# Kernel optimization log

Measured on AMD Instinct MI355X. Metric: run time of the kernel, lower is better.

The kernel has to match this reference:

```python
import jax, jax.numpy as jnp
import numpy as np

N, C_IN, T, V, M = 2048, 16, 8, 21, 2
C_OUT = 64
VM = V * M                       # 42 = n_joints
NUM_NODES = N * T * VM           # 688128 flattened nodes
NUM_HEDGES = NUM_NODES           # hyperedge ids drawn from same range
E_INC = 4 * NUM_NODES            # incidence (node, hyperedge) pairs
EMBED = VM * C_OUT // 8          # 336
HEADS = 4
HEAD_DIM = EMBED // HEADS        # 84


def setup_inputs() -> dict:
    key = jax.random.key(0)
    ks = jax.random.split(key, 16)
    g = lambda k, s: jax.random.normal(k, s, jnp.float32) * 0.02
    return dict(
        x=jax.random.normal(ks[0], (N, C_IN, T, V, M), jnp.float32),
        hi=jax.random.randint(ks[1], (2, E_INC), 0, NUM_NODES, jnp.int32),
        hc_w=g(ks[2], (C_OUT, C_IN)), hc_b=jnp.zeros((C_OUT,), jnp.float32),
        conv_w=g(ks[3], (8, 8)), conv_b=jnp.zeros((8,), jnp.float32),
        bn_gamma=jnp.ones((C_IN,), jnp.float32), bn_beta=jnp.zeros((C_IN,), jnp.float32),
        proj_w=g(ks[4], (C_OUT, C_IN)), proj_b=jnp.zeros((C_OUT,), jnp.float32),
        wq=g(ks[5], (EMBED, EMBED)), bq=jnp.zeros((EMBED,), jnp.float32),
        wk=g(ks[6], (EMBED, EMBED)), bk=jnp.zeros((EMBED,), jnp.float32),
        wv=g(ks[7], (EMBED, EMBED)), bv=jnp.zeros((EMBED,), jnp.float32),
        in_proj_w=g(ks[8], (3 * EMBED, EMBED)), in_proj_b=jnp.zeros((3 * EMBED,), jnp.float32),
        out_proj_w=g(ks[9], (EMBED, EMBED)), out_proj_b=jnp.zeros((EMBED,), jnp.float32),
        fc_w=g(ks[10], (8 * EMBED, EMBED)), fc_b=jnp.zeros((8 * EMBED,), jnp.float32),
    )


def _forward(x, hi, hc_w, hc_b, conv_w, conv_b, bn_gamma, bn_beta, proj_w, proj_b,
             wq, bq, wk, bk, wv, bv, in_proj_w, in_proj_b, out_proj_w, out_proj_b,
             fc_w, fc_b):
    # ---- residual branch: rearrange n c t v m -> n c (vm) t, BN (train-mode batch stats), proj ----
    res = x.reshape(N, C_IN, T, VM).transpose(0, 1, 3, 2)          # [N,C,VM,T]
    mean = res.mean(axis=(0, 2, 3), keepdims=True)
    var = ((res - mean) ** 2).mean(axis=(0, 2, 3), keepdims=True)
    res = (res - mean) * jax.lax.rsqrt(var + 1e-5)
    res = res * bn_gamma[None, :, None, None] + bn_beta[None, :, None, None]
    res = res.transpose(0, 3, 2, 1)                                 # n t vm c
    res = res @ proj_w.T + proj_b                                   # [N,T,VM,C_OUT]
    res = res.reshape(N, T, VM * C_OUT)                             # [N,8,2688]

    # ---- HypergraphConv (PyG math: D^-1 H B H^T X Theta + bias) ----
    xn = x.transpose(0, 2, 3, 4, 1).reshape(NUM_NODES, C_IN)        # (n t v m) c
    xt = xn @ hc_w.T                                                # [Nn, C_OUT]
    node_idx, edge_idx = hi[0], hi[1]
    ones = jnp.ones((E_INC,), xt.dtype)
    D = jax.ops.segment_sum(ones, node_idx, NUM_NODES)
    Dinv = jnp.where(D > 0, 1.0 / D, 0.0)
    Bd = jax.ops.segment_sum(ones, edge_idx, NUM_HEDGES)
    Binv = jnp.where(Bd > 0, 1.0 / Bd, 0.0)
    e = jax.ops.segment_sum(Binv[edge_idx, None] * xt[node_idx], edge_idx, NUM_HEDGES)
    h = jax.ops.segment_sum(Dinv[node_idx, None] * e[edge_idx], node_idx, NUM_NODES)
    h = h + hc_b                                                    # [Nn, C_OUT]

    # torch .view(N,-1,T,V,M) is a raw reshape of the (nodes, C) buffer
    h = h.reshape(N, C_OUT, T, V, M)
    h = h.transpose(0, 2, 3, 4, 1).reshape(N, T, VM, C_OUT)         # n t vm c

    # ---- Conv2d(8->8, k=(1,1), stride=(1,8)) over channel dim T ----
    hs = h[:, :, :, ::8]                                            # [N,8,VM,8]
    hc2 = jnp.einsum('oi,nivw->novw', conv_w, hs) + conv_b[None, :, None, None]
    seq = hc2.transpose(0, 1, 3, 2).reshape(N, 8, EMBED)            # n t (c vm) -> [N,8,336]

    # ---- external QKV projections + nn.MultiheadAttention ----
    q = seq @ wq.T + bq
    k = seq @ wk.T + bk
    v = seq @ wv.T + bv
    qq = q @ in_proj_w[:EMBED].T + in_proj_b[:EMBED]
    kk = k @ in_proj_w[EMBED:2 * EMBED].T + in_proj_b[EMBED:2 * EMBED]
    vv = v @ in_proj_w[2 * EMBED:].T + in_proj_b[2 * EMBED:]
    qq = qq.reshape(N, 8, HEADS, HEAD_DIM)
    kk = kk.reshape(N, 8, HEADS, HEAD_DIM)
    vv = vv.reshape(N, 8, HEADS, HEAD_DIM)
    scores = jnp.einsum('nshd,nthd->nhst', qq, kk) / np.sqrt(HEAD_DIM).astype(np.float32)
    attn = jax.nn.softmax(scores, axis=-1)
    ao = jnp.einsum('nhst,nthd->nshd', attn, vv).reshape(N, 8, EMBED)
    ao = ao @ out_proj_w.T + out_proj_b

    out = ao @ fc_w.T + fc_b                                        # [N,8,8*EMBED=2688]
    out = jax.nn.relu(out + res)
    return out.reshape(N, 64, T, V, M)                              # raw view, C'=64


def reference(x, hi, hc_w, hc_b, conv_w, conv_b, bn_gamma, bn_beta, proj_w, proj_b,
              wq, bq, wk, bk, wv, bv, in_proj_w, in_proj_b, out_proj_w, out_proj_b,
              fc_w, fc_b):
    return _forward(x, hi, hc_w, hc_b, conv_w, conv_b, bn_gamma, bn_beta, proj_w, proj_b,
                    wq, bq, wk, bk, wv, bv, in_proj_w, in_proj_b, out_proj_w, out_proj_b,
                    fc_w, fc_b)
```

## Files before the change

kernel.cpp:

```cpp
#include <hip/hip_runtime.h>

#define N_    2048
#define CIN   16
#define T_    8
#define VM_   42
#define COUT  64
#define NODES (N_*T_*VM_)
#define EINC  (4*NODES)
#define EMB   336
#define PERN  (T_*VM_*COUT)
#define XPERN (CIN*T_*VM_)
#define NBUK  672
#define BCAP  4608
#define LCAP  16

typedef __attribute__((ext_vector_type(8))) short bf16x8;
typedef __attribute__((ext_vector_type(4))) float f32x4;
typedef unsigned short ushort_t;
typedef unsigned char  uchar_t;

static const size_t O_A   = 0;
static const size_t SZ_AB = (size_t)NODES*64;
static const size_t O_B   = SZ_AB;
static const size_t O_SEQ = 2*SZ_AB;
static const size_t SZ_SEQ= (size_t)N_*8*EMB;
static const size_t O_AO  = O_SEQ+SZ_SEQ;
static const size_t O_SD  = O_AO+SZ_SEQ;
static const size_t O_BN  = O_SD + 4*(size_t)NODES;
static const size_t O_BE  = O_BN + 64;
static const size_t O_WF  = O_BE + 4096;
static const size_t O_SEQF = O_B;
static const size_t O_AOF  = O_B + 3600000;
static const size_t O_QKV  = O_B + 6600000;

__device__ inline short bf16r(float f){
    unsigned u = __builtin_bit_cast(unsigned, f);
    u += 0x7FFFu + ((u>>16)&1u);
    return (short)(u>>16);
}
__device__ inline float b2f(ushort_t u){
    return __builtin_bit_cast(float, ((unsigned)u)<<16);
}
__device__ inline uchar_t f2fp8(float f){
    return (uchar_t)(__builtin_amdgcn_cvt_pk_fp8_f32(f,f,0,false)&0xFFu);
}

__global__ __launch_bounds__(256) void k_bn_stats(const float* __restrict__ x, float* __restrict__ bn){
    int b=blockIdx.x, ci=b&15, grp=b>>4;
    int w=threadIdx.x>>6, lane=threadIdx.x&63;
    float s=0.f,q=0.f;
    for(int i=0;i<16;i++){
        int n = grp*64 + w*16 + i;
        const float4* r4 = (const float4*)(x + (size_t)n*XPERN + ci*336);
        for(int k=lane;k<84;k+=64){
            float4 v=r4[k];
            s += v.x+v.y+v.z+v.w;
            q += v.x*v.x+v.y*v.y+v.z*v.z+v.w*v.w;
        }
    }
    for(int off=32;off;off>>=1){ s+=__shfl_down(s,off); q+=__shfl_down(q,off); }
    if(lane==0){ atomicAdd(bn+ci,s); atomicAdd(bn+16+ci,q); }
}

__global__ void k_bn_final(float* bn, const float* __restrict__ g, const float* __restrict__ b){
    int c = threadIdx.x;
    if(c<16){
        const float inv = 1.f/(float)NODES;
        float mean = bn[c]*inv;
        float var  = bn[16+c]*inv - mean*mean;
        float rs   = rsqrtf(var+1e-5f);
        float sc   = g[c]*rs;
        bn[32+c] = sc;
        bn[48+c] = b[c]-mean*sc;
    }
}

__global__ __launch_bounds__(256) void k_xt(const float* __restrict__ x, const float* __restrict__ hcw, uchar_t* __restrict__ xt){
    __shared__ float xs[5376];
    int n=blockIdx.x, tid=threadIdx.x;
    const float4* xr4=(const float4*)(x+(size_t)n*XPERN);
    float4* xs4=(float4*)xs;
    for(int f=tid; f<1344; f+=256) xs4[f]=xr4[f];
    int co=tid&63, q=tid>>6;
    float w[16];
    #pragma unroll
    for(int ci=0;ci<16;ci++) w[ci]=hcw[co*16+ci];
    __syncthreads();
    uchar_t* xn = xt + (size_t)n*336*64;
    for(int g=0; g<21; g++){
        int tl0 = q*84 + g*4;
        float4 acc={0.f,0.f,0.f,0.f};
        #pragma unroll
        for(int ci=0;ci<16;ci++){
            float4 xv = *(const float4*)(xs + ci*336 + tl0);
            acc.x+=xv.x*w[ci]; acc.y+=xv.y*w[ci]; acc.z+=xv.z*w[ci]; acc.w+=xv.w*w[ci];
        }
        xn[(size_t)(tl0+0)*64+co]=f2fp8(acc.x);
        xn[(size_t)(tl0+1)*64+co]=f2fp8(acc.y);
        xn[(size_t)(tl0+2)*64+co]=f2fp8(acc.z);
        xn[(size_t)(tl0+3)*64+co]=f2fp8(acc.w);
    }
}

__global__ void k_initcur(int* __restrict__ gcurE, int* __restrict__ gcurD){
    int i=blockIdx.x*256+threadIdx.x;
    if(i<NBUK){ gcurE[i]=i*BCAP; gcurD[i]=i*BCAP; }
}

__global__ __launch_bounds__(256) void k_bin(const int* __restrict__ seg, const int* __restrict__ pay,
                                             int* __restrict__ gcur, unsigned* __restrict__ staging){
    __shared__ unsigned bins[NBUK*LCAP];
    __shared__ int lcnt[NBUK];
    int tid=threadIdx.x;
    for(int i=tid;i<NBUK;i+=256) lcnt[i]=0;
    __syncthreads();
    int base=blockIdx.x*4096;
    for(int k=0;k<16;k++){
        int i=base+k*256+tid;
        int sv=seg[i], pv=pay[i];
        int b=sv>>10;
        unsigned e=((unsigned)(sv&1023)<<20)|(unsigned)pv;
        int p=atomicAdd(&lcnt[b],1);
        if(p<LCAP) bins[b*LCAP+p]=e;
        else{
            int g=atomicAdd(&gcur[b],1);
            if(g<(b+1)*BCAP) staging[g]=e;
        }
    }
    __syncthreads();
    for(int b=tid;b<NBUK;b+=256){
        int c=lcnt[b]; if(c>LCAP)c=LCAP;
        if(c>0){
            int g=atomicAdd(&gcur[b],c);
            int lim=(b+1)*BCAP;
            for(int j=0;j<c;j++) if(g+j<lim) staging[g+j]=bins[b*LCAP+j];
        }
    }
}

__global__ __launch_bounds__(256) void k_csrsort(unsigned* __restrict__ staging, const int* __restrict__ gcur,
                                                 int* __restrict__ startX, int* __restrict__ cntX){
    __shared__ unsigned ents[BCAP];
    __shared__ unsigned outp[BCAP];
    __shared__ int segc[1024];
    __shared__ int wsum[4];
    int b=blockIdx.x, tid=threadIdx.x, lane=tid&63, wv=tid>>6;
    int cnt_b = gcur[b] - b*BCAP;
    if(cnt_b>BCAP) cnt_b=BCAP;
    unsigned* sb = staging + (size_t)b*BCAP;
    for(int i=tid;i<cnt_b;i+=256) ents[i]=sb[i];
    for(int i=tid;i<1024;i+=256) segc[i]=0;
    __syncthreads();
    for(int i=tid;i<cnt_b;i+=256) atomicAdd(&segc[ents[i]>>20],1);
    __syncthreads();
    int c0=segc[tid*4],c1=segc[tid*4+1],c2=segc[tid*4+2],c3=segc[tid*4+3];
    int tsum=c0+c1+c2+c3;
    int incl=tsum;
    #pragma unroll
    for(int off=1;off<64;off<<=1){ int v=__shfl_up(incl,off); if(lane>=off) incl+=v; }
    if(lane==63) wsum[wv]=incl;
    __syncthreads();
    int w0=wsum[0],w1=wsum[1],w2=wsum[2];
    int wexcl = (wv>0?w0:0)+(wv>1?w1:0)+(wv>2?w2:0);
    int run = incl - tsum + wexcl;
    int gs = b*1024 + tid*4;
    startX[gs+0]=b*BCAP+run; cntX[gs+0]=c0; segc[tid*4+0]=run; run+=c0;
    startX[gs+1]=b*BCAP+run; cntX[gs+1]=c1; segc[tid*4+1]=run; run+=c1;
    startX[gs+2]=b*BCAP+run; cntX[gs+2]=c2; segc[tid*4+2]=run; run+=c2;
    startX[gs+3]=b*BCAP+run; cntX[gs+3]=c3; segc[tid*4+3]=run; run+=c3;
    __syncthreads();
    for(int i=tid;i<cnt_b;i+=256){
        unsigned e=ents[i]; int s=e>>20;
        int p=atomicAdd(&segc[s],1);
        outp[p]=e&0xFFFFFu;
    }
    __syncthreads();
    for(int i=tid;i<cnt_b;i+=256) sb[i]=outp[i];
}

__global__ __launch_bounds__(256) void k_gath(const uchar_t* __restrict__ src, const int* __restrict__ csr,
                                              const int* __restrict__ startX, const int* __restrict__ cntX,
                                              uchar_t* __restrict__ dst){
    int s = blockIdx.x*8 + (threadIdx.x>>5);
    int l = threadIdx.x & 31;
    int c = cntX[s];
    int start = startX[s];
    float ax=0.f, ay=0.f;
    int nv = (c<32)? c : 32;
    int myidx = (l<nv)? csr[start+l] : 0;
    for(int j=0;j<nv;j++){
        int idx = __shfl(myidx, j, 32);
        unsigned v = *(const ushort_t*)(src + (size_t)idx*64 + l*2);
        ax += __builtin_amdgcn_cvt_f32_fp8(v,0);
        ay += __builtin_amdgcn_cvt_f32_fp8(v,1);
    }
    for(int j=32;j<c;j++){
        int idx = csr[start+j];
        unsigned v = *(const ushort_t*)(src + (size_t)idx*64 + l*2);
        ax += __builtin_amdgcn_cvt_f32_fp8(v,0);
        ay += __builtin_amdgcn_cvt_f32_fp8(v,1);
    }
    float scale = (c>0)? 1.f/(float)c : 0.f;
    unsigned p = __builtin_amdgcn_cvt_pk_fp8_f32(ax*scale, ay*scale, 0, false);
    *(ushort_t*)(dst + (size_t)s*64 + l*2) = (ushort_t)(p&0xFFFFu);
}

__global__ __launch_bounds__(256) void k_seq(const uchar_t* __restrict__ h,
                                             const float* __restrict__ hcb, const float* __restrict__ cw,
                                             const float* __restrict__ cb, short* __restrict__ seqf){
    __shared__ float hb[64], cws[64], cbs[8];
    int n = blockIdx.x, tid=threadIdx.x;
    if(tid<64){ hb[tid]=hcb[tid]; cws[tid]=cw[tid]; }
    if(tid<8) cbs[tid]=cb[tid];
    __syncthreads();
    const uchar_t* hn = h + (size_t)n*PERN;
    int rbase = (n&1)*8;
    short* d0 = seqf + (size_t)(n>>1)*5632;
    for(int e=tid; e<336; e+=256){
        int k = e/42, u = e%42;
        float hv[8];
        #pragma unroll
        for(int t=0;t<8;t++){
            int idx = 2688*k + t*42 + u;
            hv[t] = __builtin_amdgcn_cvt_f32_fp8((unsigned)hn[idx],0) + hb[idx&63];
        }
        int lpart = ((e>>3)&3)<<4;
        size_t obase = (size_t)(e>>5)*512 + (e&7);
        #pragma unroll
        for(int o=0;o<8;o++){
            float acc=cbs[o];
            #pragma unroll
            for(int t=0;t<8;t++) acc += cws[o*8+t]*hv[t];
            d0[obase + (size_t)((rbase+o)|lpart)*8] = bf16r(acc);
        }
    }
    if(tid<128){
        int o=tid>>4, kk=336+(tid&15);
        int l=(rbase+o)|(((kk>>3)&3)<<4);
        d0[(size_t)(kk>>5)*512 + (size_t)l*8 + (kk&7)] = 0;
    }
}

__global__ __launch_bounds__(256) void k_fusew2(const float* __restrict__ ipw, const float* __restrict__ ipb,
        const float* __restrict__ wq, const float* __restrict__ wk, const float* __restrict__ wv,
        const float* __restrict__ bq, const float* __restrict__ bk, const float* __restrict__ bv,
        const float* __restrict__ fcw, const float* __restrict__ opw,
        const float* __restrict__ opb, const float* __restrict__ fcb,
        short* __restrict__ W1F, short* __restrict__ W2F, float* __restrict__ BE){
    __shared__ float As[5376], Ws[5376], bms[336];
    int rt=blockIdx.x, r0=rt*16, tid=threadIdx.x;
    int m=(r0<1008)?(r0/336):3;
    const float* Asrc = (m<3)? (ipw+(size_t)r0*336) : (fcw+(size_t)(r0-1008)*336);
    const float* Bmat = (m==0)?wq:((m==1)?wk:((m==2)?wv:opw));
    const float* bvec = (m==0)?bq:((m==1)?bk:((m==2)?bv:opb));
    for(int f=tid;f<5376;f+=256) As[f]=Asrc[f];
    for(int f=tid;f<336;f+=256) bms[f]=bvec[f];
    __syncthreads();
    if(tid<168){
        int i0=tid, i1=tid+168;
        float a0[16], a1[16];
        #pragma unroll
        for(int r=0;r<16;r++){a0[r]=0.f;a1[r]=0.f;}
        for(int k=0;k<336;k++){
            float b0=Bmat[(size_t)k*336+i0];
            float b1=Bmat[(size_t)k*336+i1];
            #pragma unroll
            for(int r=0;r<16;r++){ float av=As[r*336+k]; a0[r]+=av*b0; a1[r]+=av*b1; }
        }
        #pragma unroll
        for(int r=0;r<16;r++){ Ws[r*336+i0]=a0[r]; Ws[r*336+i1]=a1[r]; }
    }
    if(tid>=192 && tid<208){
        int rr=tid-192;
        float acc=(m<3)? ipb[r0+rr] : fcb[r0+rr-1008];
        for(int k=0;k<336;k++) acc+=As[rr*336+k]*bms[k];
        BE[r0+rr]=acc;
    }
    __syncthreads();
    short* dst=(m<3)? (W1F+(size_t)rt*5632) : (W2F+(size_t)(rt-63)*5632);
    for(int f=tid; f<5632; f+=256){
        int kb=f>>9, rem=f&511, l=rem>>3, j=rem&7;
        int row=l&15, k=kb*32+((l>>4)<<3)+j;
        dst[f] = (k<336)? bf16r(Ws[row*336+k]) : (short)0;
    }
}

__global__ __launch_bounds__(256) void k_res(const float* __restrict__ x, const float* __restrict__ bn,
                                             const float* __restrict__ pw, const float* __restrict__ pb,
                                             const float* __restrict__ bfc, ushort_t* __restrict__ res){
    __shared__ float xp[5376], pws[1024], pbs[64], scs[16], shs[16];
    int n=blockIdx.x, tid=threadIdx.x;
    if(tid<16){ scs[tid]=bn[32+tid]; shs[tid]=bn[48+tid]; }
    if(tid<64) pbs[tid]=pb[tid];
    for(int f=tid;f<1024;f+=256) pws[f]=pw[f];
    __syncthreads();
    const float* xn = x + (size_t)n*XPERN;
    for(int f=tid;f<5376;f+=256){ int ci=f/336; xp[f]=xn[f]*scs[ci]+shs[ci]; }
    __syncthreads();
    ushort_t* rn = res + (size_t)n*PERN;
    for(int j=tid;j<2688;j+=256){
        int co=j&63, w=j>>6;
        float base = bfc[j]+pbs[co];
        float a[8];
        #pragma unroll
        for(int s=0;s<8;s++) a[s]=base;
        #pragma unroll
        for(int ci=0;ci<16;ci++){
            float c=pws[co*16+ci];
            const float* xr = xp + ci*336 + w;
            #pragma unroll
            for(int s=0;s<8;s++) a[s]+=c*xr[s*42];
        }
        #pragma unroll
        for(int s=0;s<8;s++) rn[s*2688+j]=(ushort_t)bf16r(a[s]);
    }
}

__global__ __launch_bounds__(256) void k_gemm_qkv(const bf16x8* __restrict__ Af, const bf16x8* __restrict__ Wf,
                                                  const float* __restrict__ bias, ushort_t* __restrict__ C){
    __shared__ float stage[32][68];
    int wv = threadIdx.x>>6, l = threadIdx.x&63;
    int ct = blockIdx.y*4 + wv;
    int rt0 = blockIdx.x*2;
    if(ct<63){
        const bf16x8* Ap = Af + (size_t)rt0*704 + l;
        const bf16x8* Bp = Wf + (size_t)ct *704 + l;
        f32x4 acc0={0.f,0.f,0.f,0.f}, acc1={0.f,0.f,0.f,0.f};
        #pragma unroll
        for(int kb=0;kb<11;kb++){
            bf16x8 b  = Bp[kb*64];
            bf16x8 a0 = Ap[kb*64];
            bf16x8 a1 = Ap[704 + kb*64];
            acc0 = __builtin_amdgcn_mfma_f32_16x16x32_bf16(a0,b,acc0,0,0,0);
            acc1 = __builtin_amdgcn_mfma_f32_16x16x32_bf16(a1,b,acc1,0,0,0);
        }
        int cc=wv*16+(l&15), rr0=(l>>4)*4;
        float bb = bias[ct*16+(l&15)];
        #pragma unroll
        for(int r=0;r<4;r++){
            stage[rr0+r][cc]    = acc0[r]+bb;
            stage[rr0+16+r][cc] = acc1[r]+bb;
        }
    }
    __syncthreads();
    int lr=threadIdx.x>>3, q=threadIdx.x&7;
    int col0 = blockIdx.y*64 + q*8;
    if(col0<1008){
        short u8[8];
        #pragma unroll
        for(int j=0;j<8;j++) u8[j]=bf16r(stage[lr][q*8+j]);
        *(bf16x8*)(C + (size_t)(rt0*16+lr)*1008 + col0) = *(bf16x8*)u8;
    }
}

__global__ __launch_bounds__(256) void k_gemm_out(const bf16x8* __restrict__ Af, const bf16x8* __restrict__ Wf,
                                                  const ushort_t* __restrict__ res, float* __restrict__ C){
    __shared__ float stage[32][68];
    int wv = threadIdx.x>>6, l = threadIdx.x&63;
    int ct = blockIdx.y*4 + wv;
    int rt0 = blockIdx.x*2;
    {
        const bf16x8* Ap = Af + (size_t)rt0*704 + l;
        const bf16x8* Bp = Wf + (size_t)ct *704 + l;
        f32x4 acc0={0.f,0.f,0.f,0.f}, acc1={0.f,0.f,0.f,0.f};
        #pragma unroll
        for(int kb=0;kb<11;kb++){
            bf16x8 b  = Bp[kb*64];
            bf16x8 a0 = Ap[kb*64];
            bf16x8 a1 = Ap[704 + kb*64];
            acc0 = __builtin_amdgcn_mfma_f32_16x16x32_bf16(a0,b,acc0,0,0,0);
            acc1 = __builtin_amdgcn_mfma_f32_16x16x32_bf16(a1,b,acc1,0,0,0);
        }
        int cc=wv*16+(l&15), rr0=(l>>4)*4;
        #pragma unroll
        for(int r=0;r<4;r++){
            stage[rr0+r][cc]    = acc0[r];
            stage[rr0+16+r][cc] = acc1[r];
        }
    }
    __syncthreads();
    int lr=threadIdx.x>>3, q=threadIdx.x&7;
    int row = rt0*16 + lr;
    int col0 = blockIdx.y*64 + q*8;
    bf16x8 rv = *(const bf16x8*)(res + (size_t)row*2688 + col0);
    float v[8];
    #pragma unroll
    for(int j=0;j<8;j++){
        float t = stage[lr][q*8+j] + b2f((ushort_t)rv[j]);
        v[j] = fmaxf(t,0.f);
    }
    float* dst = C + (size_t)row*2688 + col0;
    float4 f0={v[0],v[1],v[2],v[3]}, f1={v[4],v[5],v[6],v[7]};
    *(float4*)dst = f0;
    *(float4*)(dst+4) = f1;
}

__global__ __launch_bounds__(256) void k_attn2(const ushort_t* __restrict__ qkv, short* __restrict__ aof){
    __shared__ float ss[8*1008];
    __shared__ float sc[256];
    __shared__ float aos[8*336];
    int n=blockIdx.x, tid=threadIdx.x;
    const bf16x8* src8 = (const bf16x8*)(qkv + (size_t)n*8064);
    for(int i=tid; i<1008; i+=256){
        bf16x8 v = src8[i];
        #pragma unroll
        for(int j=0;j<8;j++) ss[i*8+j]=b2f((ushort_t)v[j]);
    }
    __syncthreads();
    {
        int h=tid>>6, s=(tid>>3)&7, t=tid&7;
        const float* qp=ss + s*1008 + h*84;
        const float* kp=ss + t*1008 + 336 + h*84;
        float d=0.f;
        for(int d0=0;d0<84;d0++) d+=qp[d0]*kp[d0];
        sc[tid]=d*0.10910894511799619f;
    }
    __syncthreads();
    if(tid<32){
        float* row = sc + (tid>>3)*64 + (tid&7)*8;
        float m=row[0];
        #pragma unroll
        for(int t=1;t<8;t++) m=fmaxf(m,row[t]);
        float sum=0.f;
        #pragma unroll
        for(int t=0;t<8;t++){ float e=__expf(row[t]-m); row[t]=e; sum+=e; }
        float r=1.f/sum;
        #pragma unroll
        for(int t=0;t<8;t++) row[t]*=r;
    }
    __syncthreads();
    for(int o=tid;o<336;o+=256){
        int h=o/84;
        float acc[8];
        #pragma unroll
        for(int s=0;s<8;s++) acc[s]=0.f;
        #pragma unroll
        for(int t=0;t<8;t++){
            float v=ss[t*1008+672+o];
            #pragma unroll
            for(int s=0;s<8;s++) acc[s]+=sc[h*64+s*8+t]*v;
        }
        #pragma unroll
        for(int s=0;s<8;s++) aos[s*336+o]=acc[s];
    }
    __syncthreads();
    int rt=n>>1, half=n&1;
    for(int e=tid; e<2816; e+=256){
        int row=e&7, k=e>>3;
        float v = (k<336)? aos[row*336+k] : 0.f;
        int l = (half*8+row) | (((k>>3)&3)<<4);
        int j = k&7;
        aof[(size_t)rt*5632 + (size_t)(k>>5)*512 + l*8 + j] = bf16r(v);
    }
}

extern "C" void kernel_launch(void* const* d_in, const int* in_sizes, int n_in,
                              void* d_out, int out_size, void* d_ws, size_t ws_size,
                              hipStream_t stream) {
    const float* x    = (const float*)d_in[0];
    const int*   hi   = (const int*  )d_in[1];
    const float* hcw  = (const float*)d_in[2];
    const float* hcb  = (const float*)d_in[3];
    const float* cw   = (const float*)d_in[4];
    const float* cb   = (const float*)d_in[5];
    const float* bng  = (const float*)d_in[6];
    const float* bnb  = (const float*)d_in[7];
    const float* pw   = (const float*)d_in[8];
    const float* pb   = (const float*)d_in[9];
    const float* wq   = (const float*)d_in[10];
    const float* bq   = (const float*)d_in[11];
    const float* wk   = (const float*)d_in[12];
    const float* bk   = (const float*)d_in[13];
    const float* wv   = (const float*)d_in[14];
    const float* bv   = (const float*)d_in[15];
    const float* ipw  = (const float*)d_in[16];
    const float* ipb  = (const float*)d_in[17];
    const float* opw  = (const float*)d_in[18];
    const float* opb  = (const float*)d_in[19];
    const float* fcw  = (const float*)d_in[20];
    const float* fcb  = (const float*)d_in[21];
    float* ws  = (float*)d_ws;
    float* out = (float*)d_out;

    unsigned* stgE = (unsigned*)(ws + O_SEQ);
    int* gcurE = (int*)(ws + O_SEQ) + (size_t)NBUK*BCAP;
    int* gcurD = gcurE + NBUK;
    unsigned* stgD = (unsigned*)(ws + O_AO);
    int* SD = (int*)(ws + O_SD);
    short* W1F = (short*)(ws + O_WF);
    short* W2F = W1F + (size_t)63*5632;
    ushort_t* qkvp = (ushort_t*)(ws + O_QKV);

    hipMemsetAsync(ws + O_BN, 0, 64*sizeof(float), stream);
    k_initcur<<<3,256,0,stream>>>(gcurE, gcurD);

    k_bn_stats<<<512,256,0,stream>>>(x, ws+O_BN);
    k_bn_final<<<1,64,0,stream>>>(ws+O_BN, bng, bnb);
    k_xt<<<2048,256,0,stream>>>(x, hcw, (uchar_t*)(ws+O_A));
    k_fusew2<<<231,256,0,stream>>>(ipw, ipb, wq, wk, wv, bq, bk, bv,
                                   fcw, opw, opb, fcb, W1F, W2F, ws+O_BE);

    k_bin<<<NBUK,256,0,stream>>>(hi+EINC, hi, gcurE, stgE);
    k_bin<<<NBUK,256,0,stream>>>(hi, hi+EINC, gcurD, stgD);
    k_csrsort<<<NBUK,256,0,stream>>>(stgE, gcurE, SD, SD+NODES);
    k_csrsort<<<NBUK,256,0,stream>>>(stgD, gcurD, SD+2*(size_t)NODES, SD+3*(size_t)NODES);

    k_gath<<<86016,256,0,stream>>>((const uchar_t*)(ws+O_A), (const int*)stgE,
                                   SD, SD+NODES, (uchar_t*)(ws+O_B));
    k_gath<<<86016,256,0,stream>>>((const uchar_t*)(ws+O_B), (const int*)stgD,
                                   SD+2*(size_t)NODES, SD+3*(size_t)NODES, (uchar_t*)(ws+O_A));

    k_seq<<<2048,256,0,stream>>>((const uchar_t*)(ws+O_A), hcb, cw, cb, (short*)(ws+O_SEQF));
    k_res<<<2048,256,0,stream>>>(x, ws+O_BN, pw, pb, ws+O_BE+1008, (ushort_t*)(ws+O_A));
    {   dim3 g1(512,16);
        k_gemm_qkv<<<g1,256,0,stream>>>((const bf16x8*)(ws+O_SEQF),(const bf16x8*)W1F,
                                        ws+O_BE, qkvp); }
    k_attn2<<<2048,256,0,stream>>>(qkvp, (short*)(ws+O_AOF));
    {   dim3 g2(512,42);
        k_gemm_out<<<g2,256,0,stream>>>((const bf16x8*)(ws+O_AOF),(const bf16x8*)W2F,
                                        (const ushort_t*)(ws+O_A), out); }
}
```

Baseline: 1.018 ms.

## Keep weight tiles in registers and double-buffer A rows through LDS in GEMMs

Both MFMA GEMM kernels now load each wave's 16-column weight tile into registers once and loop over 16 row tiles per block, prefetching the next A tile into a double-buffered LDS array. This is meant to cut redundant global loads of weights and A across many small blocks. The LDS-staged vectorized epilogue is replaced by direct scalar stores per lane, which may reduce store coalescing on the large fp32 output, and the grid shrinks to fewer, larger blocks.

New measurement: 938.0 us. 7.8% less time.

```diff
diff --git a/kernel.cpp b/kernel.cpp
--- a/kernel.cpp
+++ b/kernel.cpp
@@ -316,83 +316,107 @@
     }
 }
 
-__global__ __launch_bounds__(256) void k_gemm_qkv(const bf16x8* __restrict__ Af, const bf16x8* __restrict__ Wf,
+__global__ __launch_bounds__(512) void k_gemm_qkv(const bf16x8* __restrict__ Af, const bf16x8* __restrict__ Wf,
                                                   const float* __restrict__ bias, ushort_t* __restrict__ C){
-    __shared__ float stage[32][68];
-    int wv = threadIdx.x>>6, l = threadIdx.x&63;
-    int ct = blockIdx.y*4 + wv;
-    int rt0 = blockIdx.x*2;
-    if(ct<63){
-        const bf16x8* Ap = Af + (size_t)rt0*704 + l;
-        const bf16x8* Bp = Wf + (size_t)ct *704 + l;
-        f32x4 acc0={0.f,0.f,0.f,0.f}, acc1={0.f,0.f,0.f,0.f};
-        #pragma unroll
-        for(int kb=0;kb<11;kb++){
-            bf16x8 b  = Bp[kb*64];
-            bf16x8 a0 = Ap[kb*64];
-            bf16x8 a1 = Ap[704 + kb*64];
-            acc0 = __builtin_amdgcn_mfma_f32_16x16x32_bf16(a0,b,acc0,0,0,0);
-            acc1 = __builtin_amdgcn_mfma_f32_16x16x32_bf16(a1,b,acc1,0,0,0);
-        }
-        int cc=wv*16+(l&15), rr0=(l>>4)*4;
-        float bb = bias[ct*16+(l&15)];
-        #pragma unroll
-        for(int r=0;r<4;r++){
-            stage[rr0+r][cc]    = acc0[r]+bb;
-            stage[rr0+16+r][cc] = acc1[r]+bb;
-        }
-    }
-    __syncthreads();
-    int lr=threadIdx.x>>3, q=threadIdx.x&7;
-    int col0 = blockIdx.y*64 + q*8;
-    if(col0<1008){
-        short u8[8];
-        #pragma unroll
-        for(int j=0;j<8;j++) u8[j]=bf16r(stage[lr][q*8+j]);
-        *(bf16x8*)(C + (size_t)(rt0*16+lr)*1008 + col0) = *(bf16x8*)u8;
-    }
-}
-
-__global__ __launch_bounds__(256) void k_gemm_out(const bf16x8* __restrict__ Af, const bf16x8* __restrict__ Wf,
+    __shared__ short as[2][5632];
+    int tid=threadIdx.x, wid=tid>>6, l=tid&63;
+    int ct = blockIdx.y*8 + wid;
+    bool act = (ct<63);
+    bf16x8 Breg[11];
+    if(act){
+        const bf16x8* Bp = Wf + (size_t)ct*704 + l;
+        #pragma unroll
+        for(int kb=0;kb<11;kb++) Breg[kb]=Bp[kb*64];
+    }
+    float bb = act ? bias[ct*16+(l&15)] : 0.f;
+    int rt0 = blockIdx.x*16;
+    {
+        const bf16x8* src = Af + (size_t)rt0*704;
+        bf16x8 p0 = src[tid];
+        *(bf16x8*)&as[0][tid*8] = p0;
+        if(tid<192){ bf16x8 p1 = src[512+tid]; *(bf16x8*)&as[0][(512+tid)*8] = p1; }
+    }
+    __syncthreads();
+    for(int i=0;i<16;i++){
+        bf16x8 q0, q1;
+        bool pf = (i+1<16);
+        if(pf){
+            const bf16x8* src = Af + (size_t)(rt0+i+1)*704;
+            q0 = src[tid];
+            if(tid<192) q1 = src[512+tid];
+        }
+        f32x4 acc={0.f,0.f,0.f,0.f};
+        if(act){
+            const short* ab = as[i&1];
+            #pragma unroll
+            for(int kb=0;kb<11;kb++){
+                bf16x8 a = *(const bf16x8*)&ab[(kb*64+l)*8];
+                acc = __builtin_amdgcn_mfma_f32_16x16x32_bf16(a,Breg[kb],acc,0,0,0);
+            }
+            int row0 = (rt0+i)*16 + (l>>4)*4;
+            int col  = ct*16 + (l&15);
+            #pragma unroll
+            for(int rr=0;rr<4;rr++)
+                C[(size_t)(row0+rr)*1008 + col] = (ushort_t)bf16r(acc[rr]+bb);
+        }
+        if(pf){
+            *(bf16x8*)&as[(i+1)&1][tid*8] = q0;
+            if(tid<192) *(bf16x8*)&as[(i+1)&1][(512+tid)*8] = q1;
+        }
+        __syncthreads();
+    }
+}
+
+__global__ __launch_bounds__(512) void k_gemm_out(const bf16x8* __restrict__ Af, const bf16x8* __restrict__ Wf,
                                                   const ushort_t* __restrict__ res, float* __restrict__ C){
-    __shared__ float stage[32][68];
-    int wv = threadIdx.x>>6, l = threadIdx.x&63;
-    int ct = blockIdx.y*4 + wv;
-    int rt0 = blockIdx.x*2;
+    __shared__ short as[2][5632];
+    int tid=threadIdx.x, wid=tid>>6, l=tid&63;
+    int ct = blockIdx.y*8 + wid;
+    bf16x8 Breg[11];
     {
-        const bf16x8* Ap = Af + (size_t)rt0*704 + l;
-        const bf16x8* Bp = Wf + (size_t)ct *704 + l;
-        f32x4 acc0={0.f,0.f,0.f,0.f}, acc1={0.f,0.f,0.f,0.f};
-        #pragma unroll
-        for(int kb=0;kb<11;kb++){
-            bf16x8 b  = Bp[kb*64];
-            bf16x8 a0 = Ap[kb*64];
-            bf16x8 a1 = Ap[704 + kb*64];
-            acc0 = __builtin_amdgcn_mfma_f32_16x16x32_bf16(a0,b,acc0,0,0,0);
-            acc1 = __builtin_amdgcn_mfma_f32_16x16x32_bf16(a1,b,acc1,0,0,0);
-        }
-        int cc=wv*16+(l&15), rr0=(l>>4)*4;
-        #pragma unroll
-        for(int r=0;r<4;r++){
-            stage[rr0+r][cc]    = acc0[r];
-            stage[rr0+16+r][cc] = acc1[r];
-        }
-    }
-    __syncthreads();
-    int lr=threadIdx.x>>3, q=threadIdx.x&7;
-    int row = rt0*16 + lr;
-    int col0 = blockIdx.y*64 + q*8;
-    bf16x8 rv = *(const bf16x8*)(res + (size_t)row*2688 + col0);
-    float v[8];
-    #pragma unroll
-    for(int j=0;j<8;j++){
-        float t = stage[lr][q*8+j] + b2f((ushort_t)rv[j]);
-        v[j] = fmaxf(t,0.f);
-    }
-    float* dst = C + (size_t)row*2688 + col0;
-    float4 f0={v[0],v[1],v[2],v[3]}, f1={v[4],v[5],v[6],v[7]};
-    *(float4*)dst = f0;
-    *(float4*)(dst+4) = f1;
+        const bf16x8* Bp = Wf + (size_t)ct*704 + l;
+        #pragma unroll
+        for(int kb=0;kb<11;kb++) Breg[kb]=Bp[kb*64];
+    }
+    int rt0 = blockIdx.x*16;
+    {
+        const bf16x8* src = Af + (size_t)rt0*704;
+        bf16x8 p0 = src[tid];
+        *(bf16x8*)&as[0][tid*8] = p0;
+        if(tid<192){ bf16x8 p1 = src[512+tid]; *(bf16x8*)&as[0][(512+tid)*8] = p1; }
+    }
+    __syncthreads();
+    for(int i=0;i<16;i++){
+        bf16x8 q0, q1;
+        bool pf = (i+1<16);
+        if(pf){
+            const bf16x8* src = Af + (size_t)(rt0+i+1)*704;
+            q0 = src[tid];
+            if(tid<192) q1 = src[512+tid];
+        }
+        f32x4 acc={0.f,0.f,0.f,0.f};
+        {
+            const short* ab = as[i&1];
+            #pragma unroll
+            for(int kb=0;kb<11;kb++){
+                bf16x8 a = *(const bf16x8*)&ab[(kb*64+l)*8];
+                acc = __builtin_amdgcn_mfma_f32_16x16x32_bf16(a,Breg[kb],acc,0,0,0);
+            }
+            int row0 = (rt0+i)*16 + (l>>4)*4;
+            int col  = ct*16 + (l&15);
+            #pragma unroll
+            for(int rr=0;rr<4;rr++){
+                size_t o = (size_t)(row0+rr)*2688 + col;
+                float t = acc[rr] + b2f(res[o]);
+                C[o] = fmaxf(t,0.f);
+            }
+        }
+        if(pf){
+            *(bf16x8*)&as[(i+1)&1][tid*8] = q0;
+            if(tid<192) *(bf16x8*)&as[(i+1)&1][(512+tid)*8] = q1;
+        }
+        __syncthreads();
+    }
 }
 
 __global__ __launch_bounds__(256) void k_attn2(const ushort_t* __restrict__ qkv, short* __restrict__ aof){
@@ -512,11 +536,11 @@
 
     k_seq<<<2048,256,0,stream>>>((const uchar_t*)(ws+O_A), hcb, cw, cb, (short*)(ws+O_SEQF));
     k_res<<<2048,256,0,stream>>>(x, ws+O_BN, pw, pb, ws+O_BE+1008, (ushort_t*)(ws+O_A));
-    {   dim3 g1(512,16);
-        k_gemm_qkv<<<g1,256,0,stream>>>((const bf16x8*)(ws+O_SEQF),(const bf16x8*)W1F,
+    {   dim3 g1(64,8);
+        k_gemm_qkv<<<g1,512,0,stream>>>((const bf16x8*)(ws+O_SEQF),(const bf16x8*)W1F,
                                         ws+O_BE, qkvp); }
     k_attn2<<<2048,256,0,stream>>>(qkvp, (short*)(ws+O_AOF));
-    {   dim3 g2(512,42);
-        k_gemm_out<<<g2,256,0,stream>>>((const bf16x8*)(ws+O_AOF),(const bf16x8*)W2F,
+    {   dim3 g2(64,21);
+        k_gemm_out<<<g2,512,0,stream>>>((const bf16x8*)(ws+O_AOF),(const bf16x8*)W2F,
                                         (const ushort_t*)(ws+O_A), out); }
 }
```
